# Performance work log

Hardware: AMD Instinct MI355X
Metric: run time of the kernel (lower is better)

## Reference

```python
import jax, jax.numpy as jnp
import numpy as np

N_HEADS = 24
ROPE_BASE = 10000.0


def apply_rope(x, offset):
    """x: (B, H, L, Dh). Rotate pairs per RoPE (Su et al., 2021)."""
    B, H, L, Dh = x.shape
    inv_freq = 1.0 / (ROPE_BASE ** (jnp.arange(0, Dh, 2, dtype=jnp.float32) / Dh))  # (Dh/2,)
    t = jnp.arange(L, dtype=jnp.float32) + offset                                   # (L,)
    freqs = jnp.outer(t, inv_freq)                                                  # (L, Dh/2)
    emb = jnp.concatenate([freqs, freqs], axis=-1)                                  # (L, Dh)
    cos = jnp.cos(emb).astype(x.dtype)
    sin = jnp.sin(emb).astype(x.dtype)
    x1, x2 = x[..., : Dh // 2], x[..., Dh // 2 :]
    rotated = jnp.concatenate([-x2, x1], axis=-1)
    return x * cos + rotated * sin


def setup_inputs() -> dict:
    key = jax.random.key(0)
    k1, k2, k3 = jax.random.split(key, 3)
    B, L, D = 4, 2048, 1536
    x = jax.random.normal(k1, (B, L, D), dtype=jnp.float32)
    # Linear weights, torch convention (out_features, in_features), scaled init
    w_qkv = jax.random.normal(k2, (3 * D, D), dtype=jnp.float32) * 0.02
    w_out = jax.random.normal(k3, (D, D), dtype=jnp.float32) * 0.02
    return {"x": x, "w_qkv": w_qkv, "w_out": w_out, "pos_offset": 0}


def reference(x, w_qkv, w_out, pos_offset):
    B, L, D = x.shape
    H = N_HEADS
    Dh = D // H
    # fused QKV projection (no bias)
    qkv = jnp.einsum('bld,ed->ble', x, w_qkv)              # (B, L, 3D)
    qkv = qkv.reshape(B, L, 3, H, Dh)
    q = qkv[:, :, 0].transpose(0, 2, 1, 3)                 # (B, H, L, Dh)
    k = qkv[:, :, 1].transpose(0, 2, 1, 3)
    v = qkv[:, :, 2].transpose(0, 2, 1, 3)
    q = apply_rope(q, pos_offset)
    k = apply_rope(k, pos_offset)
    scale = 1.0 / np.sqrt(Dh)
    scores = jnp.einsum('bhqd,bhkd->bhqk', q, k) * scale   # (B, H, L, L)
    causal = jnp.tril(jnp.ones((L, L), dtype=bool))
    scores = jnp.where(causal, scores, jnp.finfo(scores.dtype).min)
    attn = jax.nn.softmax(scores, axis=-1)
    out = jnp.einsum('bhqk,bhkd->bhqd', attn, v)           # (B, H, L, Dh)
    out = out.transpose(0, 2, 1, 3).reshape(B, L, D)
    return jnp.einsum('bld,ed->ble', out, w_out)           # (B, L, D)
```

## Files before the change

### kernel.cpp

```cpp
#include <hip/hip_runtime.h>
#include <hip/hip_bf16.h>
#include <math.h>

typedef unsigned short u16;
typedef __bf16 b8 __attribute__((ext_vector_type(8)));
typedef __bf16 bf2t __attribute__((ext_vector_type(2)));
typedef float f4 __attribute__((ext_vector_type(4)));

#define B_ 4
#define L_ 2048
#define D_ 1536
#define H_ 24
#define DH_ 64

__device__ __forceinline__ float bf2f(u16 v) {
    union { unsigned u; float f; } z; z.u = ((unsigned)v) << 16; return z.f;
}
__device__ __forceinline__ u16 f2bf(float f) {
    union { float f; unsigned u; } z; z.f = f;
    unsigned u = z.u;
    return (u16)((u + 0x7fffu + ((u >> 16) & 1u)) >> 16);
}
__device__ __forceinline__ void f4_to_bf4(f4 v, u16 o[4]) {
#if __has_builtin(__builtin_amdgcn_cvt_pk_bf16_f32)
    union { bf2t b; unsigned u; } z0, z1;
    z0.b = __builtin_amdgcn_cvt_pk_bf16_f32(v[0], v[1]);
    z1.b = __builtin_amdgcn_cvt_pk_bf16_f32(v[2], v[3]);
    o[0] = (u16)(z0.u & 0xffffu); o[1] = (u16)(z0.u >> 16);
    o[2] = (u16)(z1.u & 0xffffu); o[3] = (u16)(z1.u >> 16);
#else
    o[0] = f2bf(v[0]); o[1] = f2bf(v[1]); o[2] = f2bf(v[2]); o[3] = f2bf(v[3]);
#endif
}

__global__ __launch_bounds__(256) void cvt3(const float* __restrict__ x,
                                            const float* __restrict__ wq,
                                            const float* __restrict__ wo,
                                            u16* __restrict__ dst,
                                            int n4x, int n4q, int n4t) {
    int i = blockIdx.x * 256 + threadIdx.x;
    if (i >= n4t) return;
    const float* src;
    int idx;
    if (i < n4x) { src = x; idx = i; }
    else if (i < n4x + n4q) { src = wq; idx = i - n4x; }
    else { src = wo; idx = i - n4x - n4q; }
    float4 vv = ((const float4*)src)[idx];
    f4 v = {vv.x, vv.y, vv.z, vv.w};
    u16 o4[4];
    f4_to_bf4(v, o4);
    ushort4 o = {o4[0], o4[1], o4[2], o4[3]};
    ((ushort4*)dst)[i] = o;
}

__global__ __launch_bounds__(256) void gemm128(const u16* __restrict__ A,
                                               const u16* __restrict__ B,
                                               float* __restrict__ Cf,
                                               u16* __restrict__ Qp,
                                               u16* __restrict__ Kp,
                                               u16* __restrict__ Vp,
                                               int M, int N, int K, int mode) {
    __shared__ u16 As[128 * 32];
    __shared__ u16 Bs[128 * 32];
    const int tid = threadIdx.x;
    const int wave = tid >> 6, lane = tid & 63;
    const int m16 = lane & 15, quad = lane >> 4;
    const int bm = blockIdx.y * 128, bn = blockIdx.x * 128;
    const int wr = (wave >> 1) * 64, wc = (wave & 1) * 64;

    f4 acc[4][4];
#pragma unroll
    for (int i = 0; i < 4; i++)
#pragma unroll
        for (int j = 0; j < 4; j++) acc[i][j] = (f4)0.0f;

    const int c0 = wave * 64 + lane;
    const int c1 = c0 + 256;
    const int r0 = c0 >> 2, col0 = (((c0 & 3) ^ ((c0 >> 2) ^ (c0 >> 4)) & 3)) * 8;
    const int r1 = c1 >> 2, col1 = (((c1 & 3) ^ ((c1 >> 2) ^ (c1 >> 4)) & 3)) * 8;
    const int fsw = (m16 ^ (m16 >> 2)) & 3;
    const int rdcol = ((quad ^ fsw) & 3) * 8;

    for (int k0 = 0; k0 < K; k0 += 32) {
        __syncthreads();
        __builtin_amdgcn_global_load_lds(
            (const __attribute__((address_space(1))) void*)(A + (size_t)(bm + r0) * K + k0 + col0),
            (__attribute__((address_space(3))) void*)(As + (size_t)c0 * 8), 16, 0, 0);
        __builtin_amdgcn_global_load_lds(
            (const __attribute__((address_space(1))) void*)(A + (size_t)(bm + r1) * K + k0 + col1),
            (__attribute__((address_space(3))) void*)(As + (size_t)c1 * 8), 16, 0, 0);
        __builtin_amdgcn_global_load_lds(
            (const __attribute__((address_space(1))) void*)(B + (size_t)(bn + r0) * K + k0 + col0),
            (__attribute__((address_space(3))) void*)(Bs + (size_t)c0 * 8), 16, 0, 0);
        __builtin_amdgcn_global_load_lds(
            (const __attribute__((address_space(1))) void*)(B + (size_t)(bn + r1) * K + k0 + col1),
            (__attribute__((address_space(3))) void*)(Bs + (size_t)c1 * 8), 16, 0, 0);
        __syncthreads();
        b8 af[4], bfm[4];
#pragma unroll
        for (int i = 0; i < 4; i++) af[i] = *(const b8*)(As + (wr + i * 16 + m16) * 32 + rdcol);
#pragma unroll
        for (int j = 0; j < 4; j++) bfm[j] = *(const b8*)(Bs + (wc + j * 16 + m16) * 32 + rdcol);
#pragma unroll
        for (int i = 0; i < 4; i++)
#pragma unroll
            for (int j = 0; j < 4; j++)
                acc[i][j] = __builtin_amdgcn_mfma_f32_16x16x32_bf16(af[i], bfm[j], acc[i][j], 0, 0, 0);
    }

    if (mode == 0) {
#pragma unroll
        for (int i = 0; i < 4; i++)
#pragma unroll
            for (int j = 0; j < 4; j++)
#pragma unroll
                for (int r = 0; r < 4; r++) {
                    int row = bm + wr + i * 16 + quad * 4 + r;
                    int col = bn + wc + j * 16 + m16;
                    Cf[(size_t)row * N + col] = acc[i][j][r];
                }
    } else {
#pragma unroll
        for (int j = 0; j < 4; j++) {
            const int colbase = bn + wc + j * 16;
            const int s = colbase / D_;
            const int h = (colbase % D_) / DH_;
            const int dh0 = colbase % DH_;
            u16* dst = (s == 0) ? Qp : ((s == 1) ? Kp : Vp);
#pragma unroll
            for (int i = 0; i < 4; i++) {
                u16 o4[4];
                f4_to_bf4(acc[i][j], o4);
#pragma unroll
                for (int r = 0; r < 4; r++) {
                    int row = bm + wr + i * 16 + quad * 4 + r;
                    int b = row >> 11, l = row & (L_ - 1);
                    dst[((size_t)(b * H_ + h) * L_ + l) * DH_ + dh0 + m16] = o4[r];
                }
            }
        }
    }
}

__global__ __launch_bounds__(256) void rope_inplace(u16* __restrict__ Qp,
                                                    u16* __restrict__ Kp,
                                                    const int* __restrict__ pos) {
    unsigned idx = blockIdx.x * 256 + threadIdx.x;
    int i = idx & 31;
    unsigned t1 = idx >> 5;
    int l = t1 & (L_ - 1);
    unsigned t2 = t1 >> 11;
    int h = t2 % H_;
    int b = t2 / H_;
    float t = (float)(l + pos[0]);
    float invf = powf(10000.0f, -(float)(2 * i) * (1.0f / 64.0f));
    float ang = t * invf;
    float c = cosf(ang), s = sinf(ang);
    size_t base = ((size_t)(b * H_ + h) * L_ + l) * DH_;
    {
        float x1 = bf2f(Qp[base + i]), x2 = bf2f(Qp[base + i + 32]);
        Qp[base + i] = f2bf((x1 * c - x2 * s) * 0.125f);
        Qp[base + i + 32] = f2bf((x2 * c + x1 * s) * 0.125f);
    }
    {
        float x1 = bf2f(Kp[base + i]), x2 = bf2f(Kp[base + i + 32]);
        Kp[base + i] = f2bf(x1 * c - x2 * s);
        Kp[base + i + 32] = f2bf(x2 * c + x1 * s);
    }
}

__global__ __launch_bounds__(256, 3) void attn(const u16* __restrict__ Q,
                                               const u16* __restrict__ K,
                                               const u16* __restrict__ V,
                                               u16* __restrict__ O) {
    __shared__ u16 Ks[64 * 72];
    __shared__ u16 Vs[64 * 72];
    __shared__ u16 Ps[4][32 * 72];
    const int tid = threadIdx.x;
    const int wave = tid >> 6, lane = tid & 63;
    const int m16 = lane & 15, quad = lane >> 4;
    const int bh = blockIdx.y;
    const int tA = blockIdx.x;
    const int tB = 15 - tA;
    const int qA = tA * 128 + wave * 32;
    const int qB = tB * 128 + wave * 32;
    const int srow = tid >> 2, scol = (tid & 3) * 16, g = (tid & 3);

    b8 qfA[2][2], qfB[2][2];
#pragma unroll
    for (int i = 0; i < 2; i++) {
        const u16* qa = Q + ((size_t)bh * L_ + qA + i * 16 + m16) * DH_;
        qfA[i][0] = *(const b8*)(qa + quad * 8);
        qfA[i][1] = *(const b8*)(qa + 32 + quad * 8);
        const u16* qb = Q + ((size_t)bh * L_ + qB + i * 16 + m16) * DH_;
        qfB[i][0] = *(const b8*)(qb + quad * 8);
        qfB[i][1] = *(const b8*)(qb + 32 + quad * 8);
    }

    float lrA[2][4], lrB[2][4];
    f4 oaccA[2][4], oaccB[2][4];
#pragma unroll
    for (int i = 0; i < 2; i++)
#pragma unroll
        for (int r = 0; r < 4; r++) { lrA[i][r] = 0.0f; lrB[i][r] = 0.0f; }
#pragma unroll
    for (int i = 0; i < 2; i++)
#pragma unroll
        for (int n = 0; n < 4; n++) { oaccA[i][n] = (f4)0.0f; oaccB[i][n] = (f4)0.0f; }

    u16* pw = Ps[wave];

    auto process = [&](int qw, b8 (&qf)[2][2], float (&lrow)[2][4], f4 (&oacc)[2][4],
                       int kbase) {
        const bool need_mask = (kbase + 64 > qw);
        f4 s[2][4];
#pragma unroll
        for (int sub = 0; sub < 4; sub++) {
            b8 k0 = *(const b8*)(Ks + (sub * 16 + m16) * 72 + quad * 8);
            b8 k1 = *(const b8*)(Ks + (sub * 16 + m16) * 72 + 32 + quad * 8);
#pragma unroll
            for (int i = 0; i < 2; i++) {
                f4 c = (f4)0.0f;
                c = __builtin_amdgcn_mfma_f32_16x16x32_bf16(qf[i][0], k0, c, 0, 0, 0);
                c = __builtin_amdgcn_mfma_f32_16x16x32_bf16(qf[i][1], k1, c, 0, 0, 0);
                s[i][sub] = c;
            }
        }
        if (need_mask) {
#pragma unroll
            for (int i = 0; i < 2; i++)
#pragma unroll
                for (int sub = 0; sub < 4; sub++)
#pragma unroll
                    for (int r = 0; r < 4; r++) {
                        const int key = kbase + sub * 16 + m16;
                        const int qg = qw + i * 16 + quad * 4 + r;
                        float p = __expf(s[i][sub][r]);
                        p = (key <= qg) ? p : 0.0f;
                        s[i][sub][r] = p;
                        lrow[i][r] += p;
                    }
        } else {
#pragma unroll
            for (int i = 0; i < 2; i++)
#pragma unroll
                for (int sub = 0; sub < 4; sub++)
#pragma unroll
                    for (int r = 0; r < 4; r++) {
                        float p = __expf(s[i][sub][r]);
                        s[i][sub][r] = p;
                        lrow[i][r] += p;
                    }
        }
#pragma unroll
        for (int i = 0; i < 2; i++)
#pragma unroll
            for (int sub = 0; sub < 4; sub++) {
                u16 o4[4];
                f4_to_bf4(s[i][sub], o4);
#pragma unroll
                for (int r = 0; r < 4; r++)
                    pw[(i * 16 + quad * 4 + r) * 72 + sub * 16 + m16] = o4[r];
            }
#pragma unroll
        for (int ks = 0; ks < 2; ks++) {
            b8 pf[2];
#pragma unroll
            for (int i = 0; i < 2; i++)
                pf[i] = *(const b8*)(pw + (i * 16 + m16) * 72 + ks * 32 + quad * 8);
#pragma unroll
            for (int n = 0; n < 4; n++) {
                b8 vf = *(const b8*)(Vs + (n * 16 + m16) * 72 +
                                     ((ks * 32 + quad * 8 + n * 16) & 63));
#pragma unroll
                for (int i = 0; i < 2; i++)
                    oacc[i][n] = __builtin_amdgcn_mfma_f32_16x16x32_bf16(pf[i], vf, oacc[i][n], 0, 0, 0);
            }
        }
    };

    const int nkt = 2 * tB + 2;
    for (int kt = 0; kt < nkt; kt++) {
        const int kbase = kt * 64;
        __syncthreads();
        {
            const u16* kg = K + ((size_t)bh * L_ + kbase + srow) * DH_ + scol;
            uint4 a0 = *(const uint4*)kg;
            uint4 a1 = *(const uint4*)(kg + 8);
            const u16* vg = V + ((size_t)bh * L_ + kbase + srow) * DH_ + scol;
            uint4 b0 = *(const uint4*)vg;
            uint4 b1 = *(const uint4*)(vg + 8);
            *(uint4*)(Ks + srow * 72 + scol) = a0;
            *(uint4*)(Ks + srow * 72 + scol + 8) = a1;
            u16 tmp[16];
            *(uint4*)(tmp) = b0;
            *(uint4*)(tmp + 8) = b1;
#pragma unroll
            for (int e = 0; e < 16; e++)
                Vs[(scol + e) * 72 + ((srow + g * 16) & 63)] = tmp[e];
        }
        __syncthreads();
        if (kbase <= qA + 31) process(qA, qfA, lrA, oaccA, kbase);
        if (kbase <= qB + 31) process(qB, qfB, lrB, oaccB, kbase);
    }

#pragma unroll
    for (int x = 1; x < 16; x <<= 1)
#pragma unroll
        for (int i = 0; i < 2; i++)
#pragma unroll
            for (int r = 0; r < 4; r++) {
                lrA[i][r] += __shfl_xor(lrA[i][r], x, 64);
                lrB[i][r] += __shfl_xor(lrB[i][r], x, 64);
            }
    const int b = bh / H_, h = bh % H_;
#pragma unroll
    for (int i = 0; i < 2; i++)
#pragma unroll
        for (int r = 0; r < 4; r++) {
            const float invA = 1.0f / lrA[i][r];
            const float invB = 1.0f / lrB[i][r];
            const int qa = qA + i * 16 + quad * 4 + r;
            const int qb = qB + i * 16 + quad * 4 + r;
#pragma unroll
            for (int n = 0; n < 4; n++) {
                O[((size_t)(b * L_ + qa)) * D_ + h * 64 + n * 16 + m16] = f2bf(oaccA[i][n][r] * invA);
                O[((size_t)(b * L_ + qb)) * D_ + h * 64 + n * 16 + m16] = f2bf(oaccB[i][n][r] * invB);
            }
        }
}

extern "C" void kernel_launch(void* const* d_in, const int* in_sizes, int n_in,
                              void* d_out, int out_size, void* d_ws, size_t ws_size,
                              hipStream_t stream) {
    const float* x = (const float*)d_in[0];
    const float* w_qkv = (const float*)d_in[1];
    const float* w_out = (const float*)d_in[2];
    const int* pos = (const int*)d_in[3];
    float* out = (float*)d_out;

    const size_t nx = (size_t)B_ * L_ * D_;
    const size_t nwq = (size_t)3 * D_ * D_;
    const size_t nwo = (size_t)D_ * D_;
    const size_t per = (size_t)B_ * H_ * L_ * DH_;

    u16* xb = (u16*)d_ws;
    u16* wqkvb = xb + nx;
    u16* woutb = wqkvb + nwq;
    u16* Qp = woutb + nwo;
    u16* Kp = Qp + per;
    u16* Vp = Kp + per;
    u16* aO = xb;

    const int n4x = (int)(nx / 4), n4q = (int)(nwq / 4), n4o = (int)(nwo / 4);
    const int n4t = n4x + n4q + n4o;
    cvt3<<<(n4t + 255) / 256, 256, 0, stream>>>(x, w_qkv, w_out, xb, n4x, n4q, n4t);

    gemm128<<<dim3(3 * D_ / 128, B_ * L_ / 128), 256, 0, stream>>>(
        xb, wqkvb, nullptr, Qp, Kp, Vp, B_ * L_, 3 * D_, D_, 1);
    rope_inplace<<<(B_ * H_ * L_ * 32) / 256, 256, 0, stream>>>(Qp, Kp, pos);
    attn<<<dim3(L_ / 256, B_ * H_), 256, 0, stream>>>(Qp, Kp, Vp, aO);
    gemm128<<<dim3(D_ / 128, B_ * L_ / 128), 256, 0, stream>>>(
        aO, woutb, out, nullptr, nullptr, nullptr, B_ * L_, D_, D_, 0);
}
```

Baseline: 527.6 us.

## Store V transposed from QKV GEMM, compute row sums via MFMA, use exp2

```diff
diff --git a/kernel.cpp b/kernel.cpp
--- a/kernel.cpp
+++ b/kernel.cpp
@@ -12,6 +12,7 @@
 #define D_ 1536
 #define H_ 24
 #define DH_ 64
+#define LOG2E 1.44269504088896f
 
 __device__ __forceinline__ float bf2f(u16 v) {
     union { unsigned u; float f; } z; z.u = ((unsigned)v) << 16; return z.f;
@@ -58,7 +59,7 @@
                                                float* __restrict__ Cf,
                                                u16* __restrict__ Qp,
                                                u16* __restrict__ Kp,
-                                               u16* __restrict__ Vp,
+                                               u16* __restrict__ Vt,
                                                int M, int N, int K, int mode) {
     __shared__ u16 As[128 * 32];
     __shared__ u16 Bs[128 * 32];
@@ -126,16 +127,28 @@
             const int s = colbase / D_;
             const int h = (colbase % D_) / DH_;
             const int dh0 = colbase % DH_;
-            u16* dst = (s == 0) ? Qp : ((s == 1) ? Kp : Vp);
-#pragma unroll
-            for (int i = 0; i < 4; i++) {
-                u16 o4[4];
-                f4_to_bf4(acc[i][j], o4);
-#pragma unroll
-                for (int r = 0; r < 4; r++) {
-                    int row = bm + wr + i * 16 + quad * 4 + r;
-                    int b = row >> 11, l = row & (L_ - 1);
-                    dst[((size_t)(b * H_ + h) * L_ + l) * DH_ + dh0 + m16] = o4[r];
+            if (s == 2) {
+#pragma unroll
+                for (int i = 0; i < 4; i++) {
+                    u16 o4[4];
+                    f4_to_bf4(acc[i][j], o4);
+                    int row = bm + wr + i * 16 + quad * 4;
+                    int b = row >> 11, l0 = row & (L_ - 1);
+                    ushort4 o = {o4[0], o4[1], o4[2], o4[3]};
+                    *(ushort4*)(Vt + ((size_t)(b * H_ + h) * DH_ + dh0 + m16) * L_ + l0) = o;
+                }
+            } else {
+                u16* dst = (s == 0) ? Qp : Kp;
+#pragma unroll
+                for (int i = 0; i < 4; i++) {
+                    u16 o4[4];
+                    f4_to_bf4(acc[i][j], o4);
+#pragma unroll
+                    for (int r = 0; r < 4; r++) {
+                        int row = bm + wr + i * 16 + quad * 4 + r;
+                        int b = row >> 11, l = row & (L_ - 1);
+                        dst[((size_t)(b * H_ + h) * L_ + l) * DH_ + dh0 + m16] = o4[r];
+                    }
                 }
             }
         }
@@ -157,10 +170,11 @@
     float ang = t * invf;
     float c = cosf(ang), s = sinf(ang);
     size_t base = ((size_t)(b * H_ + h) * L_ + l) * DH_;
+    const float qs = 0.125f * LOG2E;
     {
         float x1 = bf2f(Qp[base + i]), x2 = bf2f(Qp[base + i + 32]);
-        Qp[base + i] = f2bf((x1 * c - x2 * s) * 0.125f);
-        Qp[base + i + 32] = f2bf((x2 * c + x1 * s) * 0.125f);
+        Qp[base + i] = f2bf((x1 * c - x2 * s) * qs);
+        Qp[base + i + 32] = f2bf((x2 * c + x1 * s) * qs);
     }
     {
         float x1 = bf2f(Kp[base + i]), x2 = bf2f(Kp[base + i + 32]);
@@ -171,7 +185,7 @@
 
 __global__ __launch_bounds__(256, 3) void attn(const u16* __restrict__ Q,
                                                const u16* __restrict__ K,
-                                               const u16* __restrict__ V,
+                                               const u16* __restrict__ Vt,
                                                u16* __restrict__ O) {
     __shared__ u16 Ks[64 * 72];
     __shared__ u16 Vs[64 * 72];
@@ -184,7 +198,7 @@
     const int tB = 15 - tA;
     const int qA = tA * 128 + wave * 32;
     const int qB = tB * 128 + wave * 32;
-    const int srow = tid >> 2, scol = (tid & 3) * 16, g = (tid & 3);
+    const int srow = tid >> 2, scol = (tid & 3) * 16;
 
     b8 qfA[2][2], qfB[2][2];
 #pragma unroll
@@ -197,20 +211,26 @@
         qfB[i][1] = *(const b8*)(qb + 32 + quad * 8);
     }
 
-    float lrA[2][4], lrB[2][4];
+    b8 ones;
+    {
+        union { u16 u[8]; b8 v; } z;
+#pragma unroll
+        for (int e = 0; e < 8; e++) z.u[e] = 0x3F80;
+        ones = z.v;
+    }
+
+    f4 lA[2], lB[2];
     f4 oaccA[2][4], oaccB[2][4];
 #pragma unroll
+    for (int i = 0; i < 2; i++) { lA[i] = (f4)0.0f; lB[i] = (f4)0.0f; }
+#pragma unroll
     for (int i = 0; i < 2; i++)
 #pragma unroll
-        for (int r = 0; r < 4; r++) { lrA[i][r] = 0.0f; lrB[i][r] = 0.0f; }
-#pragma unroll
-    for (int i = 0; i < 2; i++)
-#pragma unroll
         for (int n = 0; n < 4; n++) { oaccA[i][n] = (f4)0.0f; oaccB[i][n] = (f4)0.0f; }
 
     u16* pw = Ps[wave];
 
-    auto process = [&](int qw, b8 (&qf)[2][2], float (&lrow)[2][4], f4 (&oacc)[2][4],
+    auto process = [&](int qw, b8 (&qf)[2][2], f4 (&lacc)[2], f4 (&oacc)[2][4],
                        int kbase) {
         const bool need_mask = (kbase + 64 > qw);
         f4 s[2][4];
@@ -235,10 +255,8 @@
                     for (int r = 0; r < 4; r++) {
                         const int key = kbase + sub * 16 + m16;
                         const int qg = qw + i * 16 + quad * 4 + r;
-                        float p = __expf(s[i][sub][r]);
-                        p = (key <= qg) ? p : 0.0f;
-                        s[i][sub][r] = p;
-                        lrow[i][r] += p;
+                        float p = exp2f(s[i][sub][r]);
+                        s[i][sub][r] = (key <= qg) ? p : 0.0f;
                     }
         } else {
 #pragma unroll
@@ -246,11 +264,8 @@
 #pragma unroll
                 for (int sub = 0; sub < 4; sub++)
 #pragma unroll
-                    for (int r = 0; r < 4; r++) {
-                        float p = __expf(s[i][sub][r]);
-                        s[i][sub][r] = p;
-                        lrow[i][r] += p;
-                    }
+                    for (int r = 0; r < 4; r++)
+                        s[i][sub][r] = exp2f(s[i][sub][r]);
         }
 #pragma unroll
         for (int i = 0; i < 2; i++)
@@ -266,12 +281,13 @@
         for (int ks = 0; ks < 2; ks++) {
             b8 pf[2];
 #pragma unroll
-            for (int i = 0; i < 2; i++)
+            for (int i = 0; i < 2; i++) {
                 pf[i] = *(const b8*)(pw + (i * 16 + m16) * 72 + ks * 32 + quad * 8);
+                lacc[i] = __builtin_amdgcn_mfma_f32_16x16x32_bf16(pf[i], ones, lacc[i], 0, 0, 0);
+            }
 #pragma unroll
             for (int n = 0; n < 4; n++) {
-                b8 vf = *(const b8*)(Vs + (n * 16 + m16) * 72 +
-                                     ((ks * 32 + quad * 8 + n * 16) & 63));
+                b8 vf = *(const b8*)(Vs + (n * 16 + m16) * 72 + ks * 32 + quad * 8);
 #pragma unroll
                 for (int i = 0; i < 2; i++)
                     oacc[i][n] = __builtin_amdgcn_mfma_f32_16x16x32_bf16(pf[i], vf, oacc[i][n], 0, 0, 0);
@@ -287,39 +303,26 @@
             const u16* kg = K + ((size_t)bh * L_ + kbase + srow) * DH_ + scol;
             uint4 a0 = *(const uint4*)kg;
             uint4 a1 = *(const uint4*)(kg + 8);
-            const u16* vg = V + ((size_t)bh * L_ + kbase + srow) * DH_ + scol;
+            const u16* vg = Vt + ((size_t)bh * DH_ + srow) * L_ + kbase + scol;
             uint4 b0 = *(const uint4*)vg;
             uint4 b1 = *(const uint4*)(vg + 8);
             *(uint4*)(Ks + srow * 72 + scol) = a0;
             *(uint4*)(Ks + srow * 72 + scol + 8) = a1;
-            u16 tmp[16];
-            *(uint4*)(tmp) = b0;
-            *(uint4*)(tmp + 8) = b1;
-#pragma unroll
-            for (int e = 0; e < 16; e++)
-                Vs[(scol + e) * 72 + ((srow + g * 16) & 63)] = tmp[e];
+            *(uint4*)(Vs + srow * 72 + scol) = b0;
+            *(uint4*)(Vs + srow * 72 + scol + 8) = b1;
         }
         __syncthreads();
-        if (kbase <= qA + 31) process(qA, qfA, lrA, oaccA, kbase);
-        if (kbase <= qB + 31) process(qB, qfB, lrB, oaccB, kbase);
-    }
-
-#pragma unroll
-    for (int x = 1; x < 16; x <<= 1)
-#pragma unroll
-        for (int i = 0; i < 2; i++)
-#pragma unroll
-            for (int r = 0; r < 4; r++) {
-                lrA[i][r] += __shfl_xor(lrA[i][r], x, 64);
-                lrB[i][r] += __shfl_xor(lrB[i][r], x, 64);
-            }
+        if (kbase <= qA + 31) process(qA, qfA, lA, oaccA, kbase);
+        if (kbase <= qB + 31) process(qB, qfB, lB, oaccB, kbase);
+    }
+
     const int b = bh / H_, h = bh % H_;
 #pragma unroll
     for (int i = 0; i < 2; i++)
 #pragma unroll
         for (int r = 0; r < 4; r++) {
-            const float invA = 1.0f / lrA[i][r];
-            const float invB = 1.0f / lrB[i][r];
+            const float invA = 1.0f / lA[i][r];
+            const float invB = 1.0f / lB[i][r];
             const int qa = qA + i * 16 + quad * 4 + r;
             const int qb = qB + i * 16 + quad * 4 + r;
 #pragma unroll
@@ -349,7 +352,7 @@
     u16* woutb = wqkvb + nwq;
     u16* Qp = woutb + nwo;
     u16* Kp = Qp + per;
-    u16* Vp = Kp + per;
+    u16* Vtp = Kp + per;
     u16* aO = xb;
 
     const int n4x = (int)(nx / 4), n4q = (int)(nwq / 4), n4o = (int)(nwo / 4);
@@ -357,9 +360,9 @@
     cvt3<<<(n4t + 255) / 256, 256, 0, stream>>>(x, w_qkv, w_out, xb, n4x, n4q, n4t);
 
     gemm128<<<dim3(3 * D_ / 128, B_ * L_ / 128), 256, 0, stream>>>(
-        xb, wqkvb, nullptr, Qp, Kp, Vp, B_ * L_, 3 * D_, D_, 1);
+        xb, wqkvb, nullptr, Qp, Kp, Vtp, B_ * L_, 3 * D_, D_, 1);
     rope_inplace<<<(B_ * H_ * L_ * 32) / 256, 256, 0, stream>>>(Qp, Kp, pos);
-    attn<<<dim3(L_ / 256, B_ * H_), 256, 0, stream>>>(Qp, Kp, Vp, aO);
+    attn<<<dim3(L_ / 256, B_ * H_), 256, 0, stream>>>(Qp, Kp, Vtp, aO);
     gemm128<<<dim3(D_ / 128, B_ * L_ / 128), 256, 0, stream>>>(
         aO, woutb, out, nullptr, nullptr, nullptr, B_ * L_, D_, D_, 0);
 }
```

After: 561.6 us. +6.4%, slower.
